# Kernel tuning notes

Measured on AMD Instinct MI355X. Metric: run time of the kernel, lower is better.

The kernel has to match this reference:

```python
import jax, jax.numpy as jnp
import numpy as np

V, E, DIN, DH = 8192, 4096, 512, 256
N_CLASSES = 2
EPS = 1e-5  # torch LayerNorm default
EDGE_P = 0.004  # ~33 nodes per hyperedge


def layernorm(x, g, b):
    m = jnp.mean(x, axis=-1, keepdims=True)
    v = jnp.mean((x - m) ** 2, axis=-1, keepdims=True)
    return (x - m) / jnp.sqrt(v + EPS) * g + b


def setup_inputs() -> dict:
    key = jax.random.key(0)
    ks = jax.random.split(key, 8)
    X = jax.random.normal(ks[0], (V, DIN), dtype=jnp.float32)
    # binary incidence matrix (|V|, |E|)
    H_inc = (jax.random.uniform(ks[1], (V, E)) < EDGE_P).astype(jnp.float32)
    Wp = jax.random.normal(ks[2], (DH, DIN), dtype=jnp.float32) * 0.02  # input_proj (no bias)
    W0 = jax.random.normal(ks[3], (DH, DH), dtype=jnp.float32) * 0.02
    W1 = jax.random.normal(ks[4], (DH, DH), dtype=jnp.float32) * 0.02
    g0 = jnp.ones((DH,), jnp.float32); b0 = jnp.zeros((DH,), jnp.float32)
    g1 = jnp.ones((DH,), jnp.float32); b1 = jnp.zeros((DH,), jnp.float32)
    Wc = jax.random.normal(ks[5], (N_CLASSES, DH), dtype=jnp.float32) * 0.02
    bc = jnp.zeros((N_CLASSES,), jnp.float32)
    return {"X": X, "H_inc": H_inc, "Wp": Wp, "W0": W0, "W1": W1,
            "g0": g0, "b0": b0, "g1": g1, "b1": b1, "Wc": Wc, "bc": bc}


def reference(X, H_inc, Wp, W0, W1, g0, b0, g1, b1, Wc, bc):
    # --- normalized incidence: H_tilde = D_v^{-1/2} H D_e^{-1/2}, 0 for isolated ---
    d_v = H_inc.sum(axis=1)   # (V,)
    d_e = H_inc.sum(axis=0)   # (E,)
    dvi = jnp.where(d_v > 0, jnp.where(d_v > 0, d_v, 1.0) ** -0.5, 0.0)
    dei = jnp.where(d_e > 0, jnp.where(d_e > 0, d_e, 1.0) ** -0.5, 0.0)
    H_tilde = dvi[:, None] * H_inc * dei[None, :]            # (V, E)
    HHt = H_tilde @ H_tilde.T                                # (V, V)

    # input projection
    Xh = X @ Wp.T                                            # (V, DH)

    # L=2 message-passing layers with residual + LayerNorm
    for W, g, b in ((W0, g0, b0), (W1, g1, b1)):
        Xn = jax.nn.relu((HHt @ Xh) @ W.T)
        Xh = layernorm(Xh + Xn, g, b)

    # mean pool per hyperedge (== Python loop over E in the original):
    # z_e = mean of member node embeddings; zeros for empty hyperedges
    cnt = jnp.where(d_e > 0, d_e, 1.0)[:, None]              # (E, 1)
    z_E = (H_inc.T @ Xh) / cnt                               # (E, DH)

    logits = z_E @ Wc.T + bc                                 # (E, 2)
    return jax.nn.softmax(logits, axis=1)
```

## Files before the change

kernel.cpp:

```cpp
#include <hip/hip_runtime.h>
#include <math.h>

#define NV 8192
#define NE 4096
#define DIN 512
#define DH 256
#define CAP_E 96
#define CAP_V 64
#define NPROJ (NV / 32)
#define NSCAN (NV / 2)

#define OFF_XH   0
#define OFF_UB   (OFF_XH + NV*DH)
#define OFF_YB   (OFF_UB + NV*DH/2)
#define OFF_NCNT (OFF_YB + NE*DH/2)
#define OFF_ECNT (OFF_NCNT + NV)
#define OFF_EL   (OFF_ECNT + NE*16)
#define OFF_NL   (OFF_EL + NE*CAP_E)
#define OFF_XHB  (OFF_NL + NV*CAP_V)

using bf16x8 = __attribute__((ext_vector_type(8))) short;
using f32x4  = __attribute__((ext_vector_type(4))) float;
using f32x4v = __attribute__((ext_vector_type(4))) float;

__device__ inline unsigned short f2bf(float f) {
    union { float f; unsigned u; } v; v.f = f;
    unsigned r = v.u + 0x7FFF + ((v.u >> 16) & 1);
    return (unsigned short)(r >> 16);
}
__device__ inline float b2f(unsigned short s) {
    union { unsigned u; float f; } v; v.u = ((unsigned)s) << 16; return v.f;
}

__global__ __launch_bounds__(256) void scan_proj(const float* __restrict__ H,
                                                 const float* __restrict__ X,
                                                 const float* __restrict__ Wp,
                                                 float* __restrict__ Xh,
                                                 unsigned short* __restrict__ Xhb,
                                                 int* __restrict__ edge_cnt,
                                                 int* __restrict__ node_cnt,
                                                 int* __restrict__ edge_list,
                                                 int* __restrict__ node_list) {
    __shared__ short AsBs[1024 + 8192];
    const int tid = threadIdx.x;
    if (blockIdx.x >= NPROJ) {
        const int w = tid >> 6, lane = tid & 63;
        const int v    = (blockIdx.x - NPROJ) * 2 + (w >> 1);
        const int half = w & 1;
        const f32x4v* H4 = (const f32x4v*)(H + (size_t)v * NE) + half * 512;
        f32x4v h[8];
#pragma unroll
        for (int it = 0; it < 8; ++it)
            h[it] = __builtin_nontemporal_load(&H4[lane + 64 * it]);
        unsigned m = 0u;
#pragma unroll
        for (int it = 0; it < 8; ++it) {
#pragma unroll
            for (int c = 0; c < 4; ++c)
                m |= (h[it][c] != 0.0f ? 1u : 0u) << (it * 4 + c);
        }
        int n = __builtin_popcount(m);
        int pre = n;
#pragma unroll
        for (int o = 1; o < 64; o <<= 1) {
            int t = __shfl_up(pre, o, 64);
            if (lane >= o) pre += t;
        }
        int total = __shfl(pre, 63, 64);
        int local = pre - n;
        int base = 0;
        if (lane == 0 && total > 0) base = atomicAdd(&node_cnt[v], total);
        base = __shfl(base, 0, 64) + local;
        const int ebase = half * 2048 + 4 * lane;
        int e_arr[4] = {0, 0, 0, 0};
        {
            unsigned mm = m;
#pragma unroll
            for (int u = 0; u < 4; ++u) {
                if (mm) {
                    int j = __builtin_ctz(mm);
                    mm &= mm - 1;
                    e_arr[u] = ebase + 256 * (j >> 2) + (j & 3);
                }
            }
        }
        int s_arr[4];
#pragma unroll
        for (int u = 0; u < 4; ++u)
            s_arr[u] = (u < n) ? atomicAdd(&edge_cnt[e_arr[u] << 4], 1) : 0;
#pragma unroll
        for (int u = 0; u < 4; ++u) {
            if (u < n) {
                if (s_arr[u] < CAP_E) edge_list[e_arr[u] * CAP_E + s_arr[u]] = v;
                int idx = base + u;
                if (idx < CAP_V) node_list[v * CAP_V + idx] = e_arr[u];
            }
        }
        if (n > 4) {
            unsigned mm = m;
            mm &= mm - 1; mm &= mm - 1; mm &= mm - 1; mm &= mm - 1;
            int k = 4;
            while (mm) {
                int j = __builtin_ctz(mm); mm &= mm - 1;
                int ee = ebase + 256 * (j >> 2) + (j & 3);
                int gc = atomicAdd(&edge_cnt[ee << 4], 1);
                if (gc < CAP_E) edge_list[ee * CAP_E + gc] = v;
                int idx = base + k;
                if (idx < CAP_V) node_list[v * CAP_V + idx] = ee;
                ++k;
            }
        }
        return;
    }
    short* As = AsBs;
    short* Bs = AsBs + 1024;
    const int K = DIN;
    const int lane = tid & 63;
    const int w    = tid >> 6;
    const int bm   = blockIdx.x * 32;
    const int swz  = lane ^ ((lane >> 3) & 6);
    float4 ar, br[8];
    ar = *(const float4*)(X + (size_t)(bm + (tid >> 3)) * K + ((tid & 7) << 2));
#pragma unroll
    for (int it = 0; it < 8; ++it) {
        int i = tid + it * 256;
        br[it] = *(const float4*)(Wp + (size_t)(i >> 3) * K + ((i & 7) << 2));
    }
    f32x4 acc[2][4];
#pragma unroll
    for (int mi = 0; mi < 2; ++mi)
#pragma unroll
        for (int ni = 0; ni < 4; ++ni) acc[mi][ni] = (f32x4){0.f, 0.f, 0.f, 0.f};
    for (int k0 = 0; k0 < K; k0 += 32) {
        __syncthreads();
        {
            int row = tid >> 3, kk = (tid & 7) << 2;
            int quad = kk >> 3, j = kk & 7;
            int ln = (row & 15) + (quad << 4);
            int pp = ln ^ ((ln >> 3) & 6);
            ushort4 u = {f2bf(ar.x), f2bf(ar.y), f2bf(ar.z), f2bf(ar.w)};
            *(ushort4*)&As[(row >> 4) * 512 + pp * 8 + j] = u;
        }
#pragma unroll
        for (int it = 0; it < 8; ++it) {
            int i = tid + it * 256;
            int row = i >> 3, kk = (i & 7) << 2;
            int quad = kk >> 3, j = kk & 7;
            int ln = (row & 15) + (quad << 4);
            int pp = ln ^ ((ln >> 3) & 6);
            float4 v = br[it];
            ushort4 u = {f2bf(v.x), f2bf(v.y), f2bf(v.z), f2bf(v.w)};
            *(ushort4*)&Bs[(row >> 4) * 512 + pp * 8 + j] = u;
        }
        __syncthreads();
        if (k0 + 32 < K) {
            int kn = k0 + 32;
            ar = *(const float4*)(X + (size_t)(bm + (tid >> 3)) * K + kn + ((tid & 7) << 2));
#pragma unroll
            for (int it = 0; it < 8; ++it) {
                int i = tid + it * 256;
                br[it] = *(const float4*)(Wp + (size_t)(i >> 3) * K + kn + ((i & 7) << 2));
            }
        }
        bf16x8 af[2], bfr[4];
        af[0] = *(const bf16x8*)&As[0 * 512 + swz * 8];
        af[1] = *(const bf16x8*)&As[1 * 512 + swz * 8];
#pragma unroll
        for (int ni = 0; ni < 4; ++ni)
            bfr[ni] = *(const bf16x8*)&Bs[(w * 4 + ni) * 512 + swz * 8];
#pragma unroll
        for (int mi = 0; mi < 2; ++mi)
#pragma unroll
            for (int ni = 0; ni < 4; ++ni)
                acc[mi][ni] = __builtin_amdgcn_mfma_f32_16x16x32_bf16(
                    af[mi], bfr[ni], acc[mi][ni], 0, 0, 0);
    }
    const int quad = lane >> 4, cl = lane & 15;
#pragma unroll
    for (int mi = 0; mi < 2; ++mi)
#pragma unroll
        for (int ni = 0; ni < 4; ++ni)
#pragma unroll
            for (int r = 0; r < 4; ++r) {
                float v = acc[mi][ni][r];
                size_t idx = (size_t)(bm + mi * 16 + quad * 4 + r) * DH + w * 64 + ni * 16 + cl;
                Xh[idx] = v;
                Xhb[idx] = f2bf(v);
            }
}

__global__ __launch_bounds__(256) void gemm_u(const unsigned short* __restrict__ A,
                                              const float* __restrict__ W,
                                              unsigned short* __restrict__ U) {
    const int K = DH;
    __shared__ short As[2048];
    __shared__ short Bs[16384];
    const int tid  = threadIdx.x;
    const int lane = tid & 63;
    const int w    = tid >> 6;
    const int bm   = blockIdx.x * 32;
    const int swz  = lane ^ ((lane >> 3) & 6);

    uint4 ar; float4 br[16];
    ar = *(const uint4*)(A + (size_t)(bm + (tid >> 3)) * K + ((tid & 7) << 3));
#pragma unroll
    for (int it = 0; it < 16; ++it) {
        int i = tid + it * 256;
        br[it] = *(const float4*)(W + (size_t)(i >> 4) * K + ((i & 15) << 2));
    }
    f32x4 acc[2][4];
#pragma unroll
    for (int mi = 0; mi < 2; ++mi)
#pragma unroll
        for (int ni = 0; ni < 4; ++ni) acc[mi][ni] = (f32x4){0.f, 0.f, 0.f, 0.f};

    for (int k0 = 0; k0 < K; k0 += 64) {
        __syncthreads();
        {
            int row = tid >> 3, kq = tid & 7;
            int kc = kq >> 2, quad = kq & 3;
            int ln = (row & 15) + (quad << 4);
            int pp = ln ^ ((ln >> 3) & 6);
            *(uint4*)&As[((row >> 4) * 2 + kc) * 512 + pp * 8] = ar;
        }
#pragma unroll
        for (int it = 0; it < 16; ++it) {
            int i = tid + it * 256;
            int row = i >> 4, kk = (i & 15) << 2;
            int kc = kk >> 5, quad = (kk >> 3) & 3, j = kk & 7;
            int ln = (row & 15) + (quad << 4);
            int pp = ln ^ ((ln >> 3) & 6);
            float4 v = br[it];
            ushort4 u = {f2bf(v.x), f2bf(v.y), f2bf(v.z), f2bf(v.w)};
            *(ushort4*)&Bs[((row >> 4) * 2 + kc) * 512 + pp * 8 + j] = u;
        }
        __syncthreads();
        if (k0 + 64 < K) {
            int kn = k0 + 64;
            ar = *(const uint4*)(A + (size_t)(bm + (tid >> 3)) * K + kn + ((tid & 7) << 3));
#pragma unroll
            for (int it = 0; it < 16; ++it) {
                int i = tid + it * 256;
                br[it] = *(const float4*)(W + (size_t)(i >> 4) * K + kn + ((i & 15) << 2));
            }
        }
#pragma unroll
        for (int kc = 0; kc < 2; ++kc) {
            bf16x8 af[2], bfr[4];
            af[0] = *(const bf16x8*)&As[(0 * 2 + kc) * 512 + swz * 8];
            af[1] = *(const bf16x8*)&As[(1 * 2 + kc) * 512 + swz * 8];
#pragma unroll
            for (int ni = 0; ni < 4; ++ni)
                bfr[ni] = *(const bf16x8*)&Bs[((w * 4 + ni) * 2 + kc) * 512 + swz * 8];
#pragma unroll
            for (int mi = 0; mi < 2; ++mi)
#pragma unroll
                for (int ni = 0; ni < 4; ++ni)
                    acc[mi][ni] = __builtin_amdgcn_mfma_f32_16x16x32_bf16(
                        af[mi], bfr[ni], acc[mi][ni], 0, 0, 0);
        }
    }
    const int quad = lane >> 4, cl = lane & 15;
#pragma unroll
    for (int mi = 0; mi < 2; ++mi)
#pragma unroll
        for (int ni = 0; ni < 4; ++ni)
#pragma unroll
            for (int r = 0; r < 4; ++r)
                U[(size_t)(bm + mi * 16 + quad * 4 + r) * DH + w * 64 + ni * 16 + cl]
                    = f2bf(acc[mi][ni][r]);
}

__global__ __launch_bounds__(64) void edge_gather(const unsigned short* __restrict__ Ub,
                                                  const int* __restrict__ edge_cnt,
                                                  const int* __restrict__ edge_list,
                                                  const int* __restrict__ node_cnt,
                                                  unsigned short* __restrict__ Yb) {
    int e = blockIdx.x;
    int tid = threadIdx.x;
    __shared__ int   lv[CAP_E];
    __shared__ float lc[CAP_E];
    int tc = edge_cnt[e << 4];
    int cnt = min(tc, CAP_E);
    for (int j = tid; j < cnt; j += 64) {
        int v = edge_list[e * CAP_E + j];
        lv[j] = v * (DH / 4);
        lc[j] = rsqrtf((float)node_cnt[v]);
    }
    __syncthreads();
    const ushort4* X4 = (const ushort4*)Ub;
    float4 a[8];
#pragma unroll
    for (int u = 0; u < 8; ++u) a[u] = (float4){0.f, 0.f, 0.f, 0.f};
    int i = 0;
    for (; i + 8 <= cnt; i += 8) {
#pragma unroll
        for (int u = 0; u < 8; ++u) {
            ushort4 h = X4[lv[i + u] + tid]; float c = lc[i + u];
            a[u].x = fmaf(c, b2f(h.x), a[u].x); a[u].y = fmaf(c, b2f(h.y), a[u].y);
            a[u].z = fmaf(c, b2f(h.z), a[u].z); a[u].w = fmaf(c, b2f(h.w), a[u].w);
        }
    }
    for (; i < cnt; ++i) {
        ushort4 h = X4[lv[i] + tid]; float c = lc[i];
        a[0].x = fmaf(c, b2f(h.x), a[0].x); a[0].y = fmaf(c, b2f(h.y), a[0].y);
        a[0].z = fmaf(c, b2f(h.z), a[0].z); a[0].w = fmaf(c, b2f(h.w), a[0].w);
    }
#pragma unroll
    for (int u = 4; u > 0; u >>= 1)
#pragma unroll
        for (int q = 0; q < u; ++q) {
            a[q].x += a[q + u].x; a[q].y += a[q + u].y;
            a[q].z += a[q + u].z; a[q].w += a[q + u].w;
        }
    float de = tc > 0 ? rsqrtf((float)tc) : 0.f;
    ushort4 o = {f2bf(de * a[0].x), f2bf(de * a[0].y),
                 f2bf(de * a[0].z), f2bf(de * a[0].w)};
    ((ushort4*)Yb)[e * (DH / 4) + tid] = o;
}

__global__ __launch_bounds__(64) void node_ln(const unsigned short* __restrict__ Yb,
                                              const int* __restrict__ node_cnt,
                                              const int* __restrict__ node_list,
                                              const int* __restrict__ edge_cnt,
                                              float* __restrict__ Xh,
                                              unsigned short* __restrict__ Xhb,
                                              const float* __restrict__ g,
                                              const float* __restrict__ b) {
    int v = blockIdx.x;
    int tid = threadIdx.x;
    __shared__ int   le[CAP_V];
    __shared__ float lc[CAP_V];
    int tc = node_cnt[v];
    int cnt = min(tc, CAP_V);
    if (tid < cnt) {
        int e = node_list[v * CAP_V + tid];
        le[tid] = e * (DH / 4);
        lc[tid] = rsqrtf((float)edge_cnt[e << 4]);
    }
    __syncthreads();
    const ushort4* Y4 = (const ushort4*)Yb;
    float4 a[8];
#pragma unroll
    for (int u = 0; u < 8; ++u) a[u] = (float4){0.f, 0.f, 0.f, 0.f};
    int i = 0;
    for (; i + 8 <= cnt; i += 8) {
#pragma unroll
        for (int u = 0; u < 8; ++u) {
            ushort4 h = Y4[le[i + u] + tid]; float c = lc[i + u];
            a[u].x = fmaf(c, b2f(h.x), a[u].x); a[u].y = fmaf(c, b2f(h.y), a[u].y);
            a[u].z = fmaf(c, b2f(h.z), a[u].z); a[u].w = fmaf(c, b2f(h.w), a[u].w);
        }
    }
    for (; i < cnt; ++i) {
        ushort4 h = Y4[le[i] + tid]; float c = lc[i];
        a[0].x = fmaf(c, b2f(h.x), a[0].x); a[0].y = fmaf(c, b2f(h.y), a[0].y);
        a[0].z = fmaf(c, b2f(h.z), a[0].z); a[0].w = fmaf(c, b2f(h.w), a[0].w);
    }
#pragma unroll
    for (int u = 4; u > 0; u >>= 1)
#pragma unroll
        for (int q = 0; q < u; ++q) {
            a[q].x += a[q + u].x; a[q].y += a[q + u].y;
            a[q].z += a[q + u].z; a[q].w += a[q + u].w;
        }
    float dv = tc > 0 ? rsqrtf((float)tc) : 0.f;
    float4 xr = ((const float4*)Xh)[v * (DH / 4) + tid];
    float x0 = xr.x + fmaxf(dv * a[0].x, 0.f);
    float x1 = xr.y + fmaxf(dv * a[0].y, 0.f);
    float x2 = xr.z + fmaxf(dv * a[0].z, 0.f);
    float x3 = xr.w + fmaxf(dv * a[0].w, 0.f);
    float s = (x0 + x1) + (x2 + x3);
    float q = fmaf(x0, x0, fmaf(x1, x1, fmaf(x2, x2, x3 * x3)));
#pragma unroll
    for (int o = 1; o < 64; o <<= 1) {
        s += __shfl_xor(s, o, 64);
        q += __shfl_xor(q, o, 64);
    }
    float m = s * (1.0f / DH);
    float var = q * (1.0f / DH) - m * m;
    float rstd = rsqrtf(var + 1e-5f);
    float4 g4 = ((const float4*)g)[tid];
    float4 b4 = ((const float4*)b)[tid];
    float4 o;
    o.x = (x0 - m) * rstd * g4.x + b4.x;
    o.y = (x1 - m) * rstd * g4.y + b4.y;
    o.z = (x2 - m) * rstd * g4.z + b4.z;
    o.w = (x3 - m) * rstd * g4.w + b4.w;
    ((float4*)Xh)[v * (DH / 4) + tid] = o;
    ushort4 ob = {f2bf(o.x), f2bf(o.y), f2bf(o.z), f2bf(o.w)};
    ((ushort4*)Xhb)[v * (DH / 4) + tid] = ob;
}

__global__ __launch_bounds__(64) void pool_classify(const unsigned short* __restrict__ Xhb,
                                                    const int* __restrict__ edge_cnt,
                                                    const int* __restrict__ edge_list,
                                                    const float* __restrict__ Wc,
                                                    const float* __restrict__ bc,
                                                    float* __restrict__ out) {
    int e = blockIdx.x;
    int tid = threadIdx.x;
    __shared__ int lv[CAP_E];
    int tc = edge_cnt[e << 4];
    int cnt = min(tc, CAP_E);
    for (int j = tid; j < cnt; j += 64) lv[j] = edge_list[e * CAP_E + j] * (DH / 4);
    __syncthreads();
    const ushort4* X4 = (const ushort4*)Xhb;
    float4 a[8];
#pragma unroll
    for (int u = 0; u < 8; ++u) a[u] = (float4){0, 0, 0, 0};
    int i = 0;
    for (; i + 8 <= cnt; i += 8) {
#pragma unroll
        for (int u = 0; u < 8; ++u) {
            ushort4 h = X4[lv[i + u] + tid];
            a[u].x += b2f(h.x); a[u].y += b2f(h.y);
            a[u].z += b2f(h.z); a[u].w += b2f(h.w);
        }
    }
    for (; i < cnt; ++i) {
        ushort4 h = X4[lv[i] + tid];
        a[0].x += b2f(h.x); a[0].y += b2f(h.y);
        a[0].z += b2f(h.z); a[0].w += b2f(h.w);
    }
#pragma unroll
    for (int u = 4; u > 0; u >>= 1)
#pragma unroll
        for (int q = 0; q < u; ++q) {
            a[q].x += a[q + u].x; a[q].y += a[q + u].y;
            a[q].z += a[q + u].z; a[q].w += a[q + u].w;
        }
    float inv = tc > 0 ? 1.0f / (float)tc : 1.0f;
    float4 val = {a[0].x * inv, a[0].y * inv, a[0].z * inv, a[0].w * inv};
    const float4* W4 = (const float4*)Wc;
    float4 w0 = W4[tid], w1 = W4[64 + tid];
    float p0 = val.x * w0.x + val.y * w0.y + val.z * w0.z + val.w * w0.w;
    float p1 = val.x * w1.x + val.y * w1.y + val.z * w1.z + val.w * w1.w;
#pragma unroll
    for (int o = 32; o > 0; o >>= 1) {
        p0 += __shfl_down(p0, o, 64);
        p1 += __shfl_down(p1, o, 64);
    }
    if (tid == 0) {
        float l0 = p0 + bc[0], l1 = p1 + bc[1];
        float mx = fmaxf(l0, l1);
        float e0 = expf(l0 - mx), e1 = expf(l1 - mx);
        float s = 1.0f / (e0 + e1);
        out[e * 2 + 0] = e0 * s;
        out[e * 2 + 1] = e1 * s;
    }
}

extern "C" void kernel_launch(void* const* d_in, const int* in_sizes, int n_in,
                              void* d_out, int out_size, void* d_ws, size_t ws_size,
                              hipStream_t stream) {
    const float* X  = (const float*)d_in[0];
    const float* H  = (const float*)d_in[1];
    const float* Wp = (const float*)d_in[2];
    const float* W0 = (const float*)d_in[3];
    const float* W1 = (const float*)d_in[4];
    const float* g0 = (const float*)d_in[5];
    const float* b0 = (const float*)d_in[6];
    const float* g1 = (const float*)d_in[7];
    const float* b1 = (const float*)d_in[8];
    const float* Wc = (const float*)d_in[9];
    const float* bc = (const float*)d_in[10];
    float* out = (float*)d_out;

    float* ws = (float*)d_ws;
    float* Xh  = ws + OFF_XH;
    unsigned short* Ub  = (unsigned short*)(ws + OFF_UB);
    unsigned short* Yb  = (unsigned short*)(ws + OFF_YB);
    int* node_cnt  = (int*)(ws + OFF_NCNT);
    int* edge_cnt  = (int*)(ws + OFF_ECNT);
    int* edge_list = (int*)(ws + OFF_EL);
    int* node_list = (int*)(ws + OFF_NL);
    unsigned short* Xhb = (unsigned short*)(ws + OFF_XHB);

    hipMemsetAsync(node_cnt, 0, (size_t)(NV + NE * 16) * sizeof(int), stream);

    scan_proj<<<NPROJ + NSCAN, 256, 0, stream>>>(H, X, Wp, Xh, Xhb,
                                                 edge_cnt, node_cnt, edge_list, node_list);

    const float* Ws[2] = {W0, W1};
    const float* gs[2] = {g0, g1};
    const float* bs[2] = {b0, b1};
    for (int l = 0; l < 2; ++l) {
        gemm_u<<<NV / 32, 256, 0, stream>>>(Xhb, Ws[l], Ub);
        edge_gather<<<NE, 64, 0, stream>>>(Ub, edge_cnt, edge_list, node_cnt, Yb);
        node_ln<<<NV, 64, 0, stream>>>(Yb, node_cnt, node_list, edge_cnt,
                                       Xh, Xhb, gs[l], bs[l]);
    }

    pool_classify<<<NE, 64, 0, stream>>>(Xhb, edge_cnt, edge_list, Wc, bc, out);
}
```

Before: 291.2 us.

## Fuse all stages into one cooperative persistent kernel with grid barriers

Replaces the eight separate kernel launches (scan/projection, per-layer GEMM, edge gather, node LayerNorm, pooling) with a single cooperative persistent kernel that walks the stages with grid-stride loops and a hand-rolled atomic grid barrier between them. W0/W1 are converted to bf16 once inside the kernel, so the per-layer GEMM reads the weights straight from global memory instead of staging them through LDS. This removes launch gaps and inter-kernel drain time. In exchange, the work is capped at the grid resident on the device, the barriers have a cost, and the simpler GEMM gives up shared-memory reuse.

```diff
diff --git a/kernel.cpp b/kernel.cpp
--- a/kernel.cpp
+++ b/kernel.cpp
@@ -7,17 +7,17 @@
 #define DH 256
 #define CAP_E 96
 #define CAP_V 64
-#define NPROJ (NV / 32)
-#define NSCAN (NV / 2)
 
 #define OFF_XH   0
 #define OFF_UB   (OFF_XH + NV*DH)
 #define OFF_YB   (OFF_UB + NV*DH/2)
 #define OFF_NCNT (OFF_YB + NE*DH/2)
 #define OFF_ECNT (OFF_NCNT + NV)
-#define OFF_EL   (OFF_ECNT + NE*16)
+#define OFF_BAR  (OFF_ECNT + NE*16)
+#define OFF_EL   (OFF_BAR + 32)
 #define OFF_NL   (OFF_EL + NE*CAP_E)
 #define OFF_XHB  (OFF_NL + NV*CAP_V)
+#define OFF_WB   (OFF_XHB + NV*DH/2)
 
 using bf16x8 = __attribute__((ext_vector_type(8))) short;
 using f32x4  = __attribute__((ext_vector_type(4))) float;
@@ -32,422 +32,427 @@
     union { unsigned u; float f; } v; v.u = ((unsigned)s) << 16; return v.f;
 }
 
-__global__ __launch_bounds__(256) void scan_proj(const float* __restrict__ H,
-                                                 const float* __restrict__ X,
-                                                 const float* __restrict__ Wp,
-                                                 float* __restrict__ Xh,
-                                                 unsigned short* __restrict__ Xhb,
-                                                 int* __restrict__ edge_cnt,
-                                                 int* __restrict__ node_cnt,
-                                                 int* __restrict__ edge_list,
-                                                 int* __restrict__ node_list) {
-    __shared__ short AsBs[1024 + 8192];
-    const int tid = threadIdx.x;
-    if (blockIdx.x >= NPROJ) {
-        const int w = tid >> 6, lane = tid & 63;
-        const int v    = (blockIdx.x - NPROJ) * 2 + (w >> 1);
-        const int half = w & 1;
-        const f32x4v* H4 = (const f32x4v*)(H + (size_t)v * NE) + half * 512;
-        f32x4v h[8];
-#pragma unroll
-        for (int it = 0; it < 8; ++it)
-            h[it] = __builtin_nontemporal_load(&H4[lane + 64 * it]);
-        unsigned m = 0u;
-#pragma unroll
-        for (int it = 0; it < 8; ++it) {
-#pragma unroll
-            for (int c = 0; c < 4; ++c)
-                m |= (h[it][c] != 0.0f ? 1u : 0u) << (it * 4 + c);
-        }
-        int n = __builtin_popcount(m);
-        int pre = n;
-#pragma unroll
-        for (int o = 1; o < 64; o <<= 1) {
-            int t = __shfl_up(pre, o, 64);
-            if (lane >= o) pre += t;
-        }
-        int total = __shfl(pre, 63, 64);
-        int local = pre - n;
-        int base = 0;
-        if (lane == 0 && total > 0) base = atomicAdd(&node_cnt[v], total);
-        base = __shfl(base, 0, 64) + local;
-        const int ebase = half * 2048 + 4 * lane;
-        int e_arr[4] = {0, 0, 0, 0};
-        {
-            unsigned mm = m;
-#pragma unroll
-            for (int u = 0; u < 4; ++u) {
-                if (mm) {
-                    int j = __builtin_ctz(mm);
-                    mm &= mm - 1;
-                    e_arr[u] = ebase + 256 * (j >> 2) + (j & 3);
-                }
-            }
-        }
-        int s_arr[4];
-#pragma unroll
-        for (int u = 0; u < 4; ++u)
-            s_arr[u] = (u < n) ? atomicAdd(&edge_cnt[e_arr[u] << 4], 1) : 0;
-#pragma unroll
-        for (int u = 0; u < 4; ++u) {
-            if (u < n) {
-                if (s_arr[u] < CAP_E) edge_list[e_arr[u] * CAP_E + s_arr[u]] = v;
-                int idx = base + u;
-                if (idx < CAP_V) node_list[v * CAP_V + idx] = e_arr[u];
-            }
-        }
-        if (n > 4) {
-            unsigned mm = m;
-            mm &= mm - 1; mm &= mm - 1; mm &= mm - 1; mm &= mm - 1;
-            int k = 4;
-            while (mm) {
-                int j = __builtin_ctz(mm); mm &= mm - 1;
-                int ee = ebase + 256 * (j >> 2) + (j & 3);
-                int gc = atomicAdd(&edge_cnt[ee << 4], 1);
-                if (gc < CAP_E) edge_list[ee * CAP_E + gc] = v;
-                int idx = base + k;
-                if (idx < CAP_V) node_list[v * CAP_V + idx] = ee;
-                ++k;
-            }
-        }
-        return;
+__device__ inline void gsync(int* bar, int nblk) {
+    __syncthreads();
+    if (threadIdx.x == 0) {
+        int g = __hip_atomic_load(&bar[16], __ATOMIC_RELAXED, __HIP_MEMORY_SCOPE_AGENT);
+        int a = __hip_atomic_fetch_add(&bar[0], 1, __ATOMIC_ACQ_REL, __HIP_MEMORY_SCOPE_AGENT);
+        if (a == nblk - 1) {
+            __hip_atomic_store(&bar[0], 0, __ATOMIC_RELAXED, __HIP_MEMORY_SCOPE_AGENT);
+            __hip_atomic_store(&bar[16], g + 1, __ATOMIC_RELEASE, __HIP_MEMORY_SCOPE_AGENT);
+        } else {
+            while (__hip_atomic_load(&bar[16], __ATOMIC_RELAXED, __HIP_MEMORY_SCOPE_AGENT) <= g)
+                __builtin_amdgcn_s_sleep(1);
+            (void)__hip_atomic_load(&bar[16], __ATOMIC_ACQUIRE, __HIP_MEMORY_SCOPE_AGENT);
+        }
     }
-    short* As = AsBs;
-    short* Bs = AsBs + 1024;
-    const int K = DIN;
-    const int lane = tid & 63;
-    const int w    = tid >> 6;
-    const int bm   = blockIdx.x * 32;
-    const int swz  = lane ^ ((lane >> 3) & 6);
-    float4 ar, br[8];
-    ar = *(const float4*)(X + (size_t)(bm + (tid >> 3)) * K + ((tid & 7) << 2));
-#pragma unroll
-    for (int it = 0; it < 8; ++it) {
-        int i = tid + it * 256;
-        br[it] = *(const float4*)(Wp + (size_t)(i >> 3) * K + ((i & 7) << 2));
-    }
-    f32x4 acc[2][4];
-#pragma unroll
-    for (int mi = 0; mi < 2; ++mi)
-#pragma unroll
-        for (int ni = 0; ni < 4; ++ni) acc[mi][ni] = (f32x4){0.f, 0.f, 0.f, 0.f};
-    for (int k0 = 0; k0 < K; k0 += 32) {
-        __syncthreads();
-        {
-            int row = tid >> 3, kk = (tid & 7) << 2;
-            int quad = kk >> 3, j = kk & 7;
-            int ln = (row & 15) + (quad << 4);
-            int pp = ln ^ ((ln >> 3) & 6);
-            ushort4 u = {f2bf(ar.x), f2bf(ar.y), f2bf(ar.z), f2bf(ar.w)};
-            *(ushort4*)&As[(row >> 4) * 512 + pp * 8 + j] = u;
-        }
-#pragma unroll
-        for (int it = 0; it < 8; ++it) {
-            int i = tid + it * 256;
-            int row = i >> 3, kk = (i & 7) << 2;
-            int quad = kk >> 3, j = kk & 7;
-            int ln = (row & 15) + (quad << 4);
-            int pp = ln ^ ((ln >> 3) & 6);
-            float4 v = br[it];
-            ushort4 u = {f2bf(v.x), f2bf(v.y), f2bf(v.z), f2bf(v.w)};
-            *(ushort4*)&Bs[(row >> 4) * 512 + pp * 8 + j] = u;
-        }
-        __syncthreads();
-        if (k0 + 32 < K) {
-            int kn = k0 + 32;
-            ar = *(const float4*)(X + (size_t)(bm + (tid >> 3)) * K + kn + ((tid & 7) << 2));
+    __syncthreads();
+}
+
+__global__ __launch_bounds__(256, 4) void hgnn_mega(
+    const float* __restrict__ X, const float* __restrict__ H,
+    const float* __restrict__ Wp, const float* __restrict__ W0,
+    const float* __restrict__ W1, const float* __restrict__ g0,
+    const float* __restrict__ b0, const float* __restrict__ g1,
+    const float* __restrict__ b1, const float* __restrict__ Wc,
+    const float* __restrict__ bc,
+    float* __restrict__ Xh, unsigned short* __restrict__ Xhb,
+    unsigned short* __restrict__ Ub, unsigned short* __restrict__ Yb,
+    unsigned short* __restrict__ Wb,
+    int* __restrict__ edge_cnt, int* __restrict__ node_cnt,
+    int* __restrict__ edge_list, int* __restrict__ node_list,
+    int* __restrict__ bar, float* __restrict__ out)
+{
+    __shared__ short smem_s[9216];
+    const int nblk = gridDim.x;
+    const int bid = blockIdx.x, tid = threadIdx.x;
+    const int w = tid >> 6, lane = tid & 63;
+
+    const int nproj = nblk >> 2;
+    if (bid < nproj) {
+        short* As = smem_s;
+        short* Bs = smem_s + 1024;
+        const int K = DIN;
+        const int swz = lane ^ ((lane >> 3) & 6);
+        for (int bt = bid; bt < NV / 32; bt += nproj) {
+            const int bm = bt * 32;
+            float4 ar, br[8];
+            ar = *(const float4*)(X + (size_t)(bm + (tid >> 3)) * K + ((tid & 7) << 2));
 #pragma unroll
             for (int it = 0; it < 8; ++it) {
                 int i = tid + it * 256;
-                br[it] = *(const float4*)(Wp + (size_t)(i >> 3) * K + kn + ((i & 7) << 2));
-            }
-        }
-        bf16x8 af[2], bfr[4];
-        af[0] = *(const bf16x8*)&As[0 * 512 + swz * 8];
-        af[1] = *(const bf16x8*)&As[1 * 512 + swz * 8];
-#pragma unroll
-        for (int ni = 0; ni < 4; ++ni)
-            bfr[ni] = *(const bf16x8*)&Bs[(w * 4 + ni) * 512 + swz * 8];
-#pragma unroll
-        for (int mi = 0; mi < 2; ++mi)
-#pragma unroll
-            for (int ni = 0; ni < 4; ++ni)
-                acc[mi][ni] = __builtin_amdgcn_mfma_f32_16x16x32_bf16(
-                    af[mi], bfr[ni], acc[mi][ni], 0, 0, 0);
+                br[it] = *(const float4*)(Wp + (size_t)(i >> 3) * K + ((i & 7) << 2));
+            }
+            f32x4 acc[2][4];
+#pragma unroll
+            for (int mi = 0; mi < 2; ++mi)
+#pragma unroll
+                for (int ni = 0; ni < 4; ++ni) acc[mi][ni] = (f32x4){0.f, 0.f, 0.f, 0.f};
+            for (int k0 = 0; k0 < K; k0 += 32) {
+                __syncthreads();
+                {
+                    int row = tid >> 3, kk = (tid & 7) << 2;
+                    int quad = kk >> 3, j = kk & 7;
+                    int ln = (row & 15) + (quad << 4);
+                    int pp = ln ^ ((ln >> 3) & 6);
+                    ushort4 u = {f2bf(ar.x), f2bf(ar.y), f2bf(ar.z), f2bf(ar.w)};
+                    *(ushort4*)&As[(row >> 4) * 512 + pp * 8 + j] = u;
+                }
+#pragma unroll
+                for (int it = 0; it < 8; ++it) {
+                    int i = tid + it * 256;
+                    int row = i >> 3, kk = (i & 7) << 2;
+                    int quad = kk >> 3, j = kk & 7;
+                    int ln = (row & 15) + (quad << 4);
+                    int pp = ln ^ ((ln >> 3) & 6);
+                    float4 v = br[it];
+                    ushort4 u = {f2bf(v.x), f2bf(v.y), f2bf(v.z), f2bf(v.w)};
+                    *(ushort4*)&Bs[(row >> 4) * 512 + pp * 8 + j] = u;
+                }
+                __syncthreads();
+                if (k0 + 32 < K) {
+                    int kn = k0 + 32;
+                    ar = *(const float4*)(X + (size_t)(bm + (tid >> 3)) * K + kn + ((tid & 7) << 2));
+#pragma unroll
+                    for (int it = 0; it < 8; ++it) {
+                        int i = tid + it * 256;
+                        br[it] = *(const float4*)(Wp + (size_t)(i >> 3) * K + kn + ((i & 7) << 2));
+                    }
+                }
+                bf16x8 af[2], bfr[4];
+                af[0] = *(const bf16x8*)&As[0 * 512 + swz * 8];
+                af[1] = *(const bf16x8*)&As[1 * 512 + swz * 8];
+#pragma unroll
+                for (int ni = 0; ni < 4; ++ni)
+                    bfr[ni] = *(const bf16x8*)&Bs[(w * 4 + ni) * 512 + swz * 8];
+#pragma unroll
+                for (int mi = 0; mi < 2; ++mi)
+#pragma unroll
+                    for (int ni = 0; ni < 4; ++ni)
+                        acc[mi][ni] = __builtin_amdgcn_mfma_f32_16x16x32_bf16(
+                            af[mi], bfr[ni], acc[mi][ni], 0, 0, 0);
+            }
+            const int quad = lane >> 4, cl = lane & 15;
+#pragma unroll
+            for (int mi = 0; mi < 2; ++mi)
+#pragma unroll
+                for (int ni = 0; ni < 4; ++ni)
+#pragma unroll
+                    for (int r = 0; r < 4; ++r) {
+                        float v = acc[mi][ni][r];
+                        size_t idx = (size_t)(bm + mi * 16 + quad * 4 + r) * DH + w * 64 + ni * 16 + cl;
+                        Xh[idx] = v;
+                        Xhb[idx] = f2bf(v);
+                    }
+        }
+        for (int idx = bid * 256 + tid; idx < 2 * DH * DH / 4; idx += nproj * 256) {
+            const float4* s4 = (const float4*)(idx < DH * DH / 4 ? W0 : W1);
+            float4 v = s4[idx & (DH * DH / 4 - 1)];
+            ushort4 u = {f2bf(v.x), f2bf(v.y), f2bf(v.z), f2bf(v.w)};
+            ((ushort4*)Wb)[idx] = u;
+        }
+    } else {
+        const int sw0 = (bid - nproj) * 4 + w;
+        const int nsw = (nblk - nproj) * 4;
+        for (int hr = sw0; hr < NV * 2; hr += nsw) {
+            const int v = hr >> 1, half = hr & 1;
+            const f32x4v* H4 = (const f32x4v*)(H + (size_t)v * NE) + half * 512;
+            f32x4v h[8];
+#pragma unroll
+            for (int it = 0; it < 8; ++it)
+                h[it] = __builtin_nontemporal_load(&H4[lane + 64 * it]);
+            unsigned m = 0u;
+#pragma unroll
+            for (int it = 0; it < 8; ++it) {
+#pragma unroll
+                for (int c = 0; c < 4; ++c)
+                    m |= (h[it][c] != 0.0f ? 1u : 0u) << (it * 4 + c);
+            }
+            int n = __builtin_popcount(m);
+            int pre = n;
+#pragma unroll
+            for (int o = 1; o < 64; o <<= 1) {
+                int t = __shfl_up(pre, o, 64);
+                if (lane >= o) pre += t;
+            }
+            int total = __shfl(pre, 63, 64);
+            int local = pre - n;
+            int base = 0;
+            if (lane == 0 && total > 0) base = atomicAdd(&node_cnt[v], total);
+            base = __shfl(base, 0, 64) + local;
+            const int ebase = half * 2048 + 4 * lane;
+            int e_arr[4] = {0, 0, 0, 0};
+            {
+                unsigned mm = m;
+#pragma unroll
+                for (int u = 0; u < 4; ++u) {
+                    if (mm) {
+                        int j = __builtin_ctz(mm);
+                        mm &= mm - 1;
+                        e_arr[u] = ebase + 256 * (j >> 2) + (j & 3);
+                    }
+                }
+            }
+            int s_arr[4];
+#pragma unroll
+            for (int u = 0; u < 4; ++u)
+                s_arr[u] = (u < n) ? atomicAdd(&edge_cnt[e_arr[u] << 4], 1) : 0;
+#pragma unroll
+            for (int u = 0; u < 4; ++u) {
+                if (u < n) {
+                    if (s_arr[u] < CAP_E) edge_list[e_arr[u] * CAP_E + s_arr[u]] = v;
+                    int idx = base + u;
+                    if (idx < CAP_V) node_list[v * CAP_V + idx] = e_arr[u];
+                }
+            }
+            if (n > 4) {
+                unsigned mm = m;
+                mm &= mm - 1; mm &= mm - 1; mm &= mm - 1; mm &= mm - 1;
+                int k = 4;
+                while (mm) {
+                    int j = __builtin_ctz(mm); mm &= mm - 1;
+                    int ee = ebase + 256 * (j >> 2) + (j & 3);
+                    int gc = atomicAdd(&edge_cnt[ee << 4], 1);
+                    if (gc < CAP_E) edge_list[ee * CAP_E + gc] = v;
+                    int idx = base + k;
+                    if (idx < CAP_V) node_list[v * CAP_V + idx] = ee;
+                    ++k;
+                }
+            }
+        }
     }
-    const int quad = lane >> 4, cl = lane & 15;
-#pragma unroll
-    for (int mi = 0; mi < 2; ++mi)
-#pragma unroll
-        for (int ni = 0; ni < 4; ++ni)
-#pragma unroll
-            for (int r = 0; r < 4; ++r) {
-                float v = acc[mi][ni][r];
-                size_t idx = (size_t)(bm + mi * 16 + quad * 4 + r) * DH + w * 64 + ni * 16 + cl;
-                Xh[idx] = v;
-                Xhb[idx] = f2bf(v);
-            }
-}
-
-__global__ __launch_bounds__(256) void gemm_u(const unsigned short* __restrict__ A,
-                                              const float* __restrict__ W,
-                                              unsigned short* __restrict__ U) {
-    const int K = DH;
-    __shared__ short As[2048];
-    __shared__ short Bs[16384];
-    const int tid  = threadIdx.x;
-    const int lane = tid & 63;
-    const int w    = tid >> 6;
-    const int bm   = blockIdx.x * 32;
-    const int swz  = lane ^ ((lane >> 3) & 6);
-
-    uint4 ar; float4 br[16];
-    ar = *(const uint4*)(A + (size_t)(bm + (tid >> 3)) * K + ((tid & 7) << 3));
-#pragma unroll
-    for (int it = 0; it < 16; ++it) {
-        int i = tid + it * 256;
-        br[it] = *(const float4*)(W + (size_t)(i >> 4) * K + ((i & 15) << 2));
+    gsync(bar, nblk);
+
+    for (int l = 0; l < 2; ++l) {
+        const unsigned short* Wl = Wb + (size_t)l * DH * DH;
+        const float* gg = l ? g1 : g0;
+        const float* bb = l ? b1 : b0;
+
+        {
+            const int r15 = lane & 15, k8 = (lane >> 4) << 3;
+            for (int t = bid; t < NV / 16; t += nblk) {
+                const int bm = t * 16;
+                f32x4 acc[4];
+#pragma unroll
+                for (int ni = 0; ni < 4; ++ni) acc[ni] = (f32x4){0.f, 0.f, 0.f, 0.f};
+                const unsigned short* Ap = Xhb + (size_t)(bm + r15) * DH + k8;
+                const unsigned short* Bp = Wl + (size_t)(w * 64 + r15) * DH + k8;
+#pragma unroll
+                for (int k0 = 0; k0 < DH; k0 += 32) {
+                    bf16x8 a = *(const bf16x8*)(Ap + k0);
+#pragma unroll
+                    for (int ni = 0; ni < 4; ++ni) {
+                        bf16x8 bfr = *(const bf16x8*)(Bp + (size_t)ni * 16 * DH + k0);
+                        acc[ni] = __builtin_amdgcn_mfma_f32_16x16x32_bf16(a, bfr, acc[ni], 0, 0, 0);
+                    }
+                }
+                const int quad = lane >> 4, cl = lane & 15;
+#pragma unroll
+                for (int ni = 0; ni < 4; ++ni)
+#pragma unroll
+                    for (int r = 0; r < 4; ++r)
+                        Ub[(size_t)(bm + quad * 4 + r) * DH + w * 64 + ni * 16 + cl]
+                            = f2bf(acc[ni][r]);
+            }
+        }
+        gsync(bar, nblk);
+
+        {
+            int* lvp = (int*)smem_s + w * 192;
+            float* lcp = (float*)((int*)smem_s + w * 192 + 96);
+            const int step = nblk * 4;
+            const int trips = (NE + step - 1) / step;
+            for (int tr = 0; tr < trips; ++tr) {
+                const int e = bid * 4 + w + tr * step;
+                const bool act = e < NE;
+                int tc = 0, cnt = 0;
+                if (act) {
+                    tc = edge_cnt[e << 4];
+                    cnt = min(tc, CAP_E);
+                    for (int j = lane; j < cnt; j += 64) {
+                        int v = edge_list[e * CAP_E + j];
+                        lvp[j] = v * (DH / 4);
+                        lcp[j] = rsqrtf((float)node_cnt[v]);
+                    }
+                }
+                __syncthreads();
+                if (act) {
+                    const ushort4* X4 = (const ushort4*)Ub;
+                    float4 a[8];
+#pragma unroll
+                    for (int u = 0; u < 8; ++u) a[u] = (float4){0.f, 0.f, 0.f, 0.f};
+                    int i = 0;
+                    for (; i + 8 <= cnt; i += 8) {
+#pragma unroll
+                        for (int u = 0; u < 8; ++u) {
+                            ushort4 h = X4[lvp[i + u] + lane]; float c = lcp[i + u];
+                            a[u].x = fmaf(c, b2f(h.x), a[u].x); a[u].y = fmaf(c, b2f(h.y), a[u].y);
+                            a[u].z = fmaf(c, b2f(h.z), a[u].z); a[u].w = fmaf(c, b2f(h.w), a[u].w);
+                        }
+                    }
+                    for (; i < cnt; ++i) {
+                        ushort4 h = X4[lvp[i] + lane]; float c = lcp[i];
+                        a[0].x = fmaf(c, b2f(h.x), a[0].x); a[0].y = fmaf(c, b2f(h.y), a[0].y);
+                        a[0].z = fmaf(c, b2f(h.z), a[0].z); a[0].w = fmaf(c, b2f(h.w), a[0].w);
+                    }
+#pragma unroll
+                    for (int u = 4; u > 0; u >>= 1)
+#pragma unroll
+                        for (int q = 0; q < u; ++q) {
+                            a[q].x += a[q + u].x; a[q].y += a[q + u].y;
+                            a[q].z += a[q + u].z; a[q].w += a[q + u].w;
+                        }
+                    float de = tc > 0 ? rsqrtf((float)tc) : 0.f;
+                    ushort4 o = {f2bf(de * a[0].x), f2bf(de * a[0].y),
+                                 f2bf(de * a[0].z), f2bf(de * a[0].w)};
+                    ((ushort4*)Yb)[e * (DH / 4) + lane] = o;
+                }
+                __syncthreads();
+            }
+        }
+        gsync(bar, nblk);
+
+        {
+            int* lep = (int*)smem_s + w * 128;
+            float* lcp = (float*)((int*)smem_s + w * 128 + 64);
+            const int step = nblk * 4;
+            const int trips = (NV + step - 1) / step;
+            for (int tr = 0; tr < trips; ++tr) {
+                const int v = bid * 4 + w + tr * step;
+                const bool act = v < NV;
+                int tc = 0, cnt = 0;
+                if (act) {
+                    tc = node_cnt[v];
+                    cnt = min(tc, CAP_V);
+                    if (lane < cnt) {
+                        int e = node_list[v * CAP_V + lane];
+                        lep[lane] = e * (DH / 4);
+                        lcp[lane] = rsqrtf((float)edge_cnt[e << 4]);
+                    }
+                }
+                __syncthreads();
+                if (act) {
+                    const ushort4* Y4 = (const ushort4*)Yb;
+                    float4 a[8];
+#pragma unroll
+                    for (int u = 0; u < 8; ++u) a[u] = (float4){0.f, 0.f, 0.f, 0.f};
+                    int i = 0;
+                    for (; i + 8 <= cnt; i += 8) {
+#pragma unroll
+                        for (int u = 0; u < 8; ++u) {
+                            ushort4 h = Y4[lep[i + u] + lane]; float c = lcp[i + u];
+                            a[u].x = fmaf(c, b2f(h.x), a[u].x); a[u].y = fmaf(c, b2f(h.y), a[u].y);
+                            a[u].z = fmaf(c, b2f(h.z), a[u].z); a[u].w = fmaf(c, b2f(h.w), a[u].w);
+                        }
+                    }
+                    for (; i < cnt; ++i) {
+                        ushort4 h = Y4[lep[i] + lane]; float c = lcp[i];
+                        a[0].x = fmaf(c, b2f(h.x), a[0].x); a[0].y = fmaf(c, b2f(h.y), a[0].y);
+                        a[0].z = fmaf(c, b2f(h.z), a[0].z); a[0].w = fmaf(c, b2f(h.w), a[0].w);
+                    }
+#pragma unroll
+                    for (int u = 4; u > 0; u >>= 1)
+#pragma unroll
+                        for (int q = 0; q < u; ++q) {
+                            a[q].x += a[q + u].x; a[q].y += a[q + u].y;
+                            a[q].z += a[q + u].z; a[q].w += a[q + u].w;
+                        }
+                    float dv = tc > 0 ? rsqrtf((float)tc) : 0.f;
+                    float4 xr = ((const float4*)Xh)[v * (DH / 4) + lane];
+                    float x0 = xr.x + fmaxf(dv * a[0].x, 0.f);
+                    float x1 = xr.y + fmaxf(dv * a[0].y, 0.f);
+                    float x2 = xr.z + fmaxf(dv * a[0].z, 0.f);
+                    float x3 = xr.w + fmaxf(dv * a[0].w, 0.f);
+                    float s = (x0 + x1) + (x2 + x3);
+                    float q = fmaf(x0, x0, fmaf(x1, x1, fmaf(x2, x2, x3 * x3)));
+#pragma unroll
+                    for (int o = 1; o < 64; o <<= 1) {
+                        s += __shfl_xor(s, o, 64);
+                        q += __shfl_xor(q, o, 64);
+                    }
+                    float m = s * (1.0f / DH);
+                    float var = q * (1.0f / DH) - m * m;
+                    float rstd = rsqrtf(var + 1e-5f);
+                    float4 g4 = ((const float4*)gg)[lane];
+                    float4 b4 = ((const float4*)bb)[lane];
+                    float4 o;
+                    o.x = (x0 - m) * rstd * g4.x + b4.x;
+                    o.y = (x1 - m) * rstd * g4.y + b4.y;
+                    o.z = (x2 - m) * rstd * g4.z + b4.z;
+                    o.w = (x3 - m) * rstd * g4.w + b4.w;
+                    ((float4*)Xh)[v * (DH / 4) + lane] = o;
+                    ushort4 ob = {f2bf(o.x), f2bf(o.y), f2bf(o.z), f2bf(o.w)};
+                    ((ushort4*)Xhb)[v * (DH / 4) + lane] = ob;
+                }
+                __syncthreads();
+            }
+        }
+        gsync(bar, nblk);
     }
-    f32x4 acc[2][4];
-#pragma unroll
-    for (int mi = 0; mi < 2; ++mi)
-#pragma unroll
-        for (int ni = 0; ni < 4; ++ni) acc[mi][ni] = (f32x4){0.f, 0.f, 0.f, 0.f};
-
-    for (int k0 = 0; k0 < K; k0 += 64) {
-        __syncthreads();
-        {
-            int row = tid >> 3, kq = tid & 7;
-            int kc = kq >> 2, quad = kq & 3;
-            int ln = (row & 15) + (quad << 4);
-            int pp = ln ^ ((ln >> 3) & 6);
-            *(uint4*)&As[((row >> 4) * 2 + kc) * 512 + pp * 8] = ar;
-        }
-#pragma unroll
-        for (int it = 0; it < 16; ++it) {
-            int i = tid + it * 256;
-            int row = i >> 4, kk = (i & 15) << 2;
-            int kc = kk >> 5, quad = (kk >> 3) & 3, j = kk & 7;
-            int ln = (row & 15) + (quad << 4);
-            int pp = ln ^ ((ln >> 3) & 6);
-            float4 v = br[it];
-            ushort4 u = {f2bf(v.x), f2bf(v.y), f2bf(v.z), f2bf(v.w)};
-            *(ushort4*)&Bs[((row >> 4) * 2 + kc) * 512 + pp * 8 + j] = u;
-        }
-        __syncthreads();
-        if (k0 + 64 < K) {
-            int kn = k0 + 64;
-            ar = *(const uint4*)(A + (size_t)(bm + (tid >> 3)) * K + kn + ((tid & 7) << 3));
-#pragma unroll
-            for (int it = 0; it < 16; ++it) {
-                int i = tid + it * 256;
-                br[it] = *(const float4*)(W + (size_t)(i >> 4) * K + kn + ((i & 15) << 2));
-            }
-        }
-#pragma unroll
-        for (int kc = 0; kc < 2; ++kc) {
-            bf16x8 af[2], bfr[4];
-            af[0] = *(const bf16x8*)&As[(0 * 2 + kc) * 512 + swz * 8];
-            af[1] = *(const bf16x8*)&As[(1 * 2 + kc) * 512 + swz * 8];
-#pragma unroll
-            for (int ni = 0; ni < 4; ++ni)
-                bfr[ni] = *(const bf16x8*)&Bs[((w * 4 + ni) * 2 + kc) * 512 + swz * 8];
-#pragma unroll
-            for (int mi = 0; mi < 2; ++mi)
-#pragma unroll
-                for (int ni = 0; ni < 4; ++ni)
-                    acc[mi][ni] = __builtin_amdgcn_mfma_f32_16x16x32_bf16(
-                        af[mi], bfr[ni], acc[mi][ni], 0, 0, 0);
-        }
-    }
-    const int quad = lane >> 4, cl = lane & 15;
-#pragma unroll
-    for (int mi = 0; mi < 2; ++mi)
-#pragma unroll
-        for (int ni = 0; ni < 4; ++ni)
-#pragma unroll
-            for (int r = 0; r < 4; ++r)
-                U[(size_t)(bm + mi * 16 + quad * 4 + r) * DH + w * 64 + ni * 16 + cl]
-                    = f2bf(acc[mi][ni][r]);
-}
-
-__global__ __launch_bounds__(64) void edge_gather(const unsigned short* __restrict__ Ub,
-                                                  const int* __restrict__ edge_cnt,
-                                                  const int* __restrict__ edge_list,
-                                                  const int* __restrict__ node_cnt,
-                                                  unsigned short* __restrict__ Yb) {
-    int e = blockIdx.x;
-    int tid = threadIdx.x;
-    __shared__ int   lv[CAP_E];
-    __shared__ float lc[CAP_E];
-    int tc = edge_cnt[e << 4];
-    int cnt = min(tc, CAP_E);
-    for (int j = tid; j < cnt; j += 64) {
-        int v = edge_list[e * CAP_E + j];
-        lv[j] = v * (DH / 4);
-        lc[j] = rsqrtf((float)node_cnt[v]);
-    }
-    __syncthreads();
-    const ushort4* X4 = (const ushort4*)Ub;
-    float4 a[8];
-#pragma unroll
-    for (int u = 0; u < 8; ++u) a[u] = (float4){0.f, 0.f, 0.f, 0.f};
-    int i = 0;
-    for (; i + 8 <= cnt; i += 8) {
-#pragma unroll
-        for (int u = 0; u < 8; ++u) {
-            ushort4 h = X4[lv[i + u] + tid]; float c = lc[i + u];
-            a[u].x = fmaf(c, b2f(h.x), a[u].x); a[u].y = fmaf(c, b2f(h.y), a[u].y);
-            a[u].z = fmaf(c, b2f(h.z), a[u].z); a[u].w = fmaf(c, b2f(h.w), a[u].w);
-        }
-    }
-    for (; i < cnt; ++i) {
-        ushort4 h = X4[lv[i] + tid]; float c = lc[i];
-        a[0].x = fmaf(c, b2f(h.x), a[0].x); a[0].y = fmaf(c, b2f(h.y), a[0].y);
-        a[0].z = fmaf(c, b2f(h.z), a[0].z); a[0].w = fmaf(c, b2f(h.w), a[0].w);
-    }
-#pragma unroll
-    for (int u = 4; u > 0; u >>= 1)
-#pragma unroll
-        for (int q = 0; q < u; ++q) {
-            a[q].x += a[q + u].x; a[q].y += a[q + u].y;
-            a[q].z += a[q + u].z; a[q].w += a[q + u].w;
-        }
-    float de = tc > 0 ? rsqrtf((float)tc) : 0.f;
-    ushort4 o = {f2bf(de * a[0].x), f2bf(de * a[0].y),
-                 f2bf(de * a[0].z), f2bf(de * a[0].w)};
-    ((ushort4*)Yb)[e * (DH / 4) + tid] = o;
-}
-
-__global__ __launch_bounds__(64) void node_ln(const unsigned short* __restrict__ Yb,
-                                              const int* __restrict__ node_cnt,
-                                              const int* __restrict__ node_list,
-                                              const int* __restrict__ edge_cnt,
-                                              float* __restrict__ Xh,
-                                              unsigned short* __restrict__ Xhb,
-                                              const float* __restrict__ g,
-                                              const float* __restrict__ b) {
-    int v = blockIdx.x;
-    int tid = threadIdx.x;
-    __shared__ int   le[CAP_V];
-    __shared__ float lc[CAP_V];
-    int tc = node_cnt[v];
-    int cnt = min(tc, CAP_V);
-    if (tid < cnt) {
-        int e = node_list[v * CAP_V + tid];
-        le[tid] = e * (DH / 4);
-        lc[tid] = rsqrtf((float)edge_cnt[e << 4]);
-    }
-    __syncthreads();
-    const ushort4* Y4 = (const ushort4*)Yb;
-    float4 a[8];
-#pragma unroll
-    for (int u = 0; u < 8; ++u) a[u] = (float4){0.f, 0.f, 0.f, 0.f};
-    int i = 0;
-    for (; i + 8 <= cnt; i += 8) {
-#pragma unroll
-        for (int u = 0; u < 8; ++u) {
-            ushort4 h = Y4[le[i + u] + tid]; float c = lc[i + u];
-            a[u].x = fmaf(c, b2f(h.x), a[u].x); a[u].y = fmaf(c, b2f(h.y), a[u].y);
-            a[u].z = fmaf(c, b2f(h.z), a[u].z); a[u].w = fmaf(c, b2f(h.w), a[u].w);
-        }
-    }
-    for (; i < cnt; ++i) {
-        ushort4 h = Y4[le[i] + tid]; float c = lc[i];
-        a[0].x = fmaf(c, b2f(h.x), a[0].x); a[0].y = fmaf(c, b2f(h.y), a[0].y);
-        a[0].z = fmaf(c, b2f(h.z), a[0].z); a[0].w = fmaf(c, b2f(h.w), a[0].w);
-    }
-#pragma unroll
-    for (int u = 4; u > 0; u >>= 1)
-#pragma unroll
-        for (int q = 0; q < u; ++q) {
-            a[q].x += a[q + u].x; a[q].y += a[q + u].y;
-            a[q].z += a[q + u].z; a[q].w += a[q + u].w;
-        }
-    float dv = tc > 0 ? rsqrtf((float)tc) : 0.f;
-    float4 xr = ((const float4*)Xh)[v * (DH / 4) + tid];
-    float x0 = xr.x + fmaxf(dv * a[0].x, 0.f);
-    float x1 = xr.y + fmaxf(dv * a[0].y, 0.f);
-    float x2 = xr.z + fmaxf(dv * a[0].z, 0.f);
-    float x3 = xr.w + fmaxf(dv * a[0].w, 0.f);
-    float s = (x0 + x1) + (x2 + x3);
-    float q = fmaf(x0, x0, fmaf(x1, x1, fmaf(x2, x2, x3 * x3)));
-#pragma unroll
-    for (int o = 1; o < 64; o <<= 1) {
-        s += __shfl_xor(s, o, 64);
-        q += __shfl_xor(q, o, 64);
-    }
-    float m = s * (1.0f / DH);
-    float var = q * (1.0f / DH) - m * m;
-    float rstd = rsqrtf(var + 1e-5f);
-    float4 g4 = ((const float4*)g)[tid];
-    float4 b4 = ((const float4*)b)[tid];
-    float4 o;
-    o.x = (x0 - m) * rstd * g4.x + b4.x;
-    o.y = (x1 - m) * rstd * g4.y + b4.y;
-    o.z = (x2 - m) * rstd * g4.z + b4.z;
-    o.w = (x3 - m) * rstd * g4.w + b4.w;
-    ((float4*)Xh)[v * (DH / 4) + tid] = o;
-    ushort4 ob = {f2bf(o.x), f2bf(o.y), f2bf(o.z), f2bf(o.w)};
-    ((ushort4*)Xhb)[v * (DH / 4) + tid] = ob;
-}
-
-__global__ __launch_bounds__(64) void pool_classify(const unsigned short* __restrict__ Xhb,
-                                                    const int* __restrict__ edge_cnt,
-                                                    const int* __restrict__ edge_list,
-                                                    const float* __restrict__ Wc,
-                                                    const float* __restrict__ bc,
-                                                    float* __restrict__ out) {
-    int e = blockIdx.x;
-    int tid = threadIdx.x;
-    __shared__ int lv[CAP_E];
-    int tc = edge_cnt[e << 4];
-    int cnt = min(tc, CAP_E);
-    for (int j = tid; j < cnt; j += 64) lv[j] = edge_list[e * CAP_E + j] * (DH / 4);
-    __syncthreads();
-    const ushort4* X4 = (const ushort4*)Xhb;
-    float4 a[8];
-#pragma unroll
-    for (int u = 0; u < 8; ++u) a[u] = (float4){0, 0, 0, 0};
-    int i = 0;
-    for (; i + 8 <= cnt; i += 8) {
-#pragma unroll
-        for (int u = 0; u < 8; ++u) {
-            ushort4 h = X4[lv[i + u] + tid];
-            a[u].x += b2f(h.x); a[u].y += b2f(h.y);
-            a[u].z += b2f(h.z); a[u].w += b2f(h.w);
-        }
-    }
-    for (; i < cnt; ++i) {
-        ushort4 h = X4[lv[i] + tid];
-        a[0].x += b2f(h.x); a[0].y += b2f(h.y);
-        a[0].z += b2f(h.z); a[0].w += b2f(h.w);
-    }
-#pragma unroll
-    for (int u = 4; u > 0; u >>= 1)
-#pragma unroll
-        for (int q = 0; q < u; ++q) {
-            a[q].x += a[q + u].x; a[q].y += a[q + u].y;
-            a[q].z += a[q + u].z; a[q].w += a[q + u].w;
-        }
-    float inv = tc > 0 ? 1.0f / (float)tc : 1.0f;
-    float4 val = {a[0].x * inv, a[0].y * inv, a[0].z * inv, a[0].w * inv};
-    const float4* W4 = (const float4*)Wc;
-    float4 w0 = W4[tid], w1 = W4[64 + tid];
-    float p0 = val.x * w0.x + val.y * w0.y + val.z * w0.z + val.w * w0.w;
-    float p1 = val.x * w1.x + val.y * w1.y + val.z * w1.z + val.w * w1.w;
-#pragma unroll
-    for (int o = 32; o > 0; o >>= 1) {
-        p0 += __shfl_down(p0, o, 64);
-        p1 += __shfl_down(p1, o, 64);
-    }
-    if (tid == 0) {
-        float l0 = p0 + bc[0], l1 = p1 + bc[1];
-        float mx = fmaxf(l0, l1);
-        float e0 = expf(l0 - mx), e1 = expf(l1 - mx);
-        float s = 1.0f / (e0 + e1);
-        out[e * 2 + 0] = e0 * s;
-        out[e * 2 + 1] = e1 * s;
+
+    {
+        int* lvp = (int*)smem_s + w * 96;
+        const int step = nblk * 4;
+        const int trips = (NE + step - 1) / step;
+        for (int tr = 0; tr < trips; ++tr) {
+            const int e = bid * 4 + w + tr * step;
+            const bool act = e < NE;
+            int tc = 0, cnt = 0;
+            if (act) {
+                tc = edge_cnt[e << 4];
+                cnt = min(tc, CAP_E);
+                for (int j = lane; j < cnt; j += 64)
+                    lvp[j] = edge_list[e * CAP_E + j] * (DH / 4);
+            }
+            __syncthreads();
+            if (act) {
+                const ushort4* X4 = (const ushort4*)Xhb;
+                float4 a[8];
+#pragma unroll
+                for (int u = 0; u < 8; ++u) a[u] = (float4){0, 0, 0, 0};
+                int i = 0;
+                for (; i + 8 <= cnt; i += 8) {
+#pragma unroll
+                    for (int u = 0; u < 8; ++u) {
+                        ushort4 h = X4[lvp[i + u] + lane];
+                        a[u].x += b2f(h.x); a[u].y += b2f(h.y);
+                        a[u].z += b2f(h.z); a[u].w += b2f(h.w);
+                    }
+                }
+                for (; i < cnt; ++i) {
+                    ushort4 h = X4[lvp[i] + lane];
+                    a[0].x += b2f(h.x); a[0].y += b2f(h.y);
+                    a[0].z += b2f(h.z); a[0].w += b2f(h.w);
+                }
+#pragma unroll
+                for (int u = 4; u > 0; u >>= 1)
+#pragma unroll
+                    for (int q = 0; q < u; ++q) {
+                        a[q].x += a[q + u].x; a[q].y += a[q + u].y;
+                        a[q].z += a[q + u].z; a[q].w += a[q + u].w;
+                    }
+                float inv = tc > 0 ? 1.0f / (float)tc : 1.0f;
+                float4 val = {a[0].x * inv, a[0].y * inv, a[0].z * inv, a[0].w * inv};
+                const float4* W4 = (const float4*)Wc;
+                float4 w0 = W4[lane], w1 = W4[64 + lane];
+                float p0 = val.x * w0.x + val.y * w0.y + val.z * w0.z + val.w * w0.w;
+                float p1 = val.x * w1.x + val.y * w1.y + val.z * w1.z + val.w * w1.w;
+#pragma unroll
+                for (int o = 32; o > 0; o >>= 1) {
+                    p0 += __shfl_down(p0, o, 64);
+                    p1 += __shfl_down(p1, o, 64);
+                }
+                if (lane == 0) {
+                    float l0 = p0 + bc[0], l1 = p1 + bc[1];
+                    float mx = fmaxf(l0, l1);
+                    float e0 = expf(l0 - mx), e1 = expf(l1 - mx);
+                    float sden = 1.0f / (e0 + e1);
+                    out[e * 2 + 0] = e0 * sden;
+                    out[e * 2 + 1] = e1 * sden;
+                }
+            }
+            __syncthreads();
+        }
     }
 }
 
@@ -473,24 +478,31 @@
     unsigned short* Yb  = (unsigned short*)(ws + OFF_YB);
     int* node_cnt  = (int*)(ws + OFF_NCNT);
     int* edge_cnt  = (int*)(ws + OFF_ECNT);
+    int* bar       = (int*)(ws + OFF_BAR);
     int* edge_list = (int*)(ws + OFF_EL);
     int* node_list = (int*)(ws + OFF_NL);
     unsigned short* Xhb = (unsigned short*)(ws + OFF_XHB);
-
-    hipMemsetAsync(node_cnt, 0, (size_t)(NV + NE * 16) * sizeof(int), stream);
-
-    scan_proj<<<NPROJ + NSCAN, 256, 0, stream>>>(H, X, Wp, Xh, Xhb,
-                                                 edge_cnt, node_cnt, edge_list, node_list);
-
-    const float* Ws[2] = {W0, W1};
-    const float* gs[2] = {g0, g1};
-    const float* bs[2] = {b0, b1};
-    for (int l = 0; l < 2; ++l) {
-        gemm_u<<<NV / 32, 256, 0, stream>>>(Xhb, Ws[l], Ub);
-        edge_gather<<<NE, 64, 0, stream>>>(Ub, edge_cnt, edge_list, node_cnt, Yb);
-        node_ln<<<NV, 64, 0, stream>>>(Yb, node_cnt, node_list, edge_cnt,
-                                       Xh, Xhb, gs[l], bs[l]);
+    unsigned short* Wb  = (unsigned short*)(ws + OFF_WB);
+
+    static int nblk = 0;
+    if (nblk == 0) {
+        int bpc = 0;
+        if (hipOccupancyMaxActiveBlocksPerMultiprocessor(&bpc, hgnn_mega, 256, 0) != hipSuccess
+            || bpc < 1)
+            bpc = 2;
+        if (bpc > 4) bpc = 4;
+        nblk = bpc * 256;
     }
 
-    pool_classify<<<NE, 64, 0, stream>>>(Xhb, edge_cnt, edge_list, Wc, bc, out);
+    hipMemsetAsync(node_cnt, 0, (size_t)(NV + NE * 16 + 32) * sizeof(int), stream);
+
+    void* args[] = {
+        (void*)&X, (void*)&H, (void*)&Wp, (void*)&W0, (void*)&W1,
+        (void*)&g0, (void*)&b0, (void*)&g1, (void*)&b1, (void*)&Wc, (void*)&bc,
+        (void*)&Xh, (void*)&Xhb, (void*)&Ub, (void*)&Yb, (void*)&Wb,
+        (void*)&edge_cnt, (void*)&node_cnt, (void*)&edge_list, (void*)&node_list,
+        (void*)&bar, (void*)&out
+    };
+    hipLaunchCooperativeKernel((void*)hgnn_mega, dim3(nblk), dim3(256),
+                               args, 0, stream);
 }
```

Result: slower. 763.0 us (+162.0%).
